# Optimization experiments

Hardware: AMD Instinct MI355X
Metric: run time of the kernel (lower is better)

## Reference

```python
import jax, jax.numpy as jnp
import numpy as np

B, S, V, D, H, F, GH, NC, L = 64, 256, 50000, 1024, 16, 4096, 100, 7, 4
DH = D // H


def _ln(x, g, b):
    m = x.mean(-1, keepdims=True)
    v = x.var(-1, keepdims=True)
    return (x - m) / jnp.sqrt(v + 1e-5) * g + b


def setup_inputs() -> dict:
    key = jax.random.key(0)
    ks = iter(jax.random.split(key, 40))
    nrm = lambda shp, s=0.02: jax.random.normal(next(ks), shp, jnp.float32) * s
    inp = {}
    inp["src"] = jax.random.randint(next(ks), (B, S), 0, V)
    inp["em_seq"] = jax.random.normal(next(ks), (B, S, 7), jnp.float32)
    inp["d_ids"] = jax.random.randint(next(ks), (B, 1), 0, B)
    inp["ut_len"] = jax.random.randint(next(ks), (B,), 1, S + 1)
    inp["emb"] = jax.random.uniform(next(ks), (V, D), jnp.float32, -0.1, 0.1)
    inp["Wqkv"] = nrm((L, 3 * D, D)); inp["bqkv"] = jnp.zeros((L, 3 * D), jnp.float32)
    inp["Wo"] = nrm((L, D, D)); inp["bo"] = jnp.zeros((L, D), jnp.float32)
    inp["W1"] = nrm((L, F, D)); inp["b1"] = jnp.zeros((L, F), jnp.float32)
    inp["W2"] = nrm((L, D, F)); inp["b2"] = jnp.zeros((L, D), jnp.float32)
    inp["ln1_g"] = jnp.ones((L, D), jnp.float32); inp["ln1_b"] = jnp.zeros((L, D), jnp.float32)
    inp["ln2_g"] = jnp.ones((L, D), jnp.float32); inp["ln2_b"] = jnp.zeros((L, D), jnp.float32)
    inp["gru_Wih"] = nrm((3 * GH, 7), 0.1); inp["gru_Whh"] = nrm((3 * GH, GH), 0.1)
    inp["gru_bih"] = jnp.zeros((3 * GH,), jnp.float32); inp["gru_bhh"] = jnp.zeros((3 * GH,), jnp.float32)
    inp["dec_W"] = jax.random.uniform(next(ks), (NC, 2 * D + GH), jnp.float32, -0.1, 0.1)
    inp["dec_b"] = jnp.zeros((NC,), jnp.float32)
    return inp


def reference(src, em_seq, d_ids, ut_len, emb, Wqkv, bqkv, Wo, bo, W1, b1, W2, b2,
              ln1_g, ln1_b, ln2_g, ln2_b, gru_Wih, gru_Whh, gru_bih, gru_bhh,
              dec_W, dec_b):
    # embedding + scale + sinusoidal positional encoding
    x = emb[src] * jnp.sqrt(jnp.float32(D))                      # [B,S,D]
    pos = jnp.arange(S, dtype=jnp.float32)[:, None]
    div = jnp.exp(jnp.arange(0, D, 2, dtype=jnp.float32) * (-jnp.log(10000.0) / D))
    pe = jnp.stack([jnp.sin(pos * div), jnp.cos(pos * div)], -1).reshape(S, D)
    x = x + pe

    causal = jnp.tril(jnp.ones((S, S), bool))
    neg = jnp.finfo(x.dtype).min
    for l in range(L):  # post-norm transformer encoder layers (PyTorch default)
        qkv = x @ Wqkv[l].T + bqkv[l]
        q, k, v = jnp.split(qkv, 3, -1)
        q = q.reshape(B, S, H, DH); k = k.reshape(B, S, H, DH); v = v.reshape(B, S, H, DH)
        sc = jnp.einsum('bqhd,bkhd->bhqk', q, k) / jnp.sqrt(jnp.float32(DH))
        sc = jnp.where(causal, sc, neg)
        a = jax.nn.softmax(sc, -1)
        o = jnp.einsum('bhqk,bkhd->bqhd', a, v).reshape(B, S, D)
        x = _ln(x + o @ Wo[l].T + bo[l], ln1_g[l], ln1_b[l])
        ff = jax.nn.relu(x @ W1[l].T + b1[l]) @ W2[l].T + b2[l]
        x = _ln(x + ff, ln2_g[l], ln2_b[l])

    # emotion GRU (PyTorch GRU equations), scan over time
    xp = jnp.einsum('bsf,gf->sbg', em_seq, gru_Wih) + gru_bih    # [S,B,3*GH]

    def step(h, xt):
        hp = h @ gru_Whh.T + gru_bhh
        xr, xz, xn = jnp.split(xt, 3, -1)
        hr, hz, hn = jnp.split(hp, 3, -1)
        r = jax.nn.sigmoid(xr + hr)
        z = jax.nn.sigmoid(xz + hz)
        n = jnp.tanh(xn + r * hn)
        h = (1.0 - z) * n + z * h
        return h, h

    _, hs = jax.lax.scan(step, jnp.zeros((B, GH), x.dtype), xp)
    emo = hs.transpose(1, 0, 2)                                  # [B,S,GH]

    # ragged gather of the 'main' utterance per dialogue + broadcast-concat
    lens = ut_len[d_ids[:, 0]]                                   # [B]
    main = x[jnp.arange(B), lens - 1]                            # [B,D]
    pair = jnp.concatenate([x, jnp.broadcast_to(main[:, None, :], (B, S, D))], -1)
    valid = (jnp.arange(S)[None, :] < lens[:, None])[..., None]
    pair = jnp.where(valid, pair, 0.0)                           # zeros beyond ut_len, as in torch loop
    dec_ip = jnp.concatenate([pair, emo], -1)                    # [B,S,2D+GH]
    return dec_ip @ dec_W.T + dec_b                              # [B,S,NC]
```

## Files before the change

### kernel.cpp

```cpp
#include <hip/hip_runtime.h>
#include <hip/hip_bf16.h>
#include <math.h>

#define BB 64
#define SS 256
#define DD 1024
#define HH 16
#define FFN 4096
#define GHH 100
#define NCC 7
#define LL 4
#define TT (BB*SS)
#define DHH 64

typedef unsigned short u16;
typedef unsigned int u32;
typedef __attribute__((ext_vector_type(4))) float f32x4;
typedef __attribute__((ext_vector_type(8))) short s16x8;
typedef __attribute__((ext_vector_type(4))) unsigned short u16x4;
typedef __attribute__((ext_vector_type(8))) unsigned short u16x8;

__device__ __forceinline__ u16 f2bf(float f) {
  union { float f; u32 u; } x; x.f = f;
  u32 r = x.u + 0x7FFFu + ((x.u >> 16) & 1u);
  return (u16)(r >> 16);
}
__device__ __forceinline__ float bf2f(u16 b) {
  union { u32 u; float f; } x; x.u = ((u32)b) << 16;
  return x.f;
}
__device__ __forceinline__ u32 pkbf(float a, float b) {
  return (u32)f2bf(a) | ((u32)f2bf(b) << 16);
}
__device__ __forceinline__ float lo16(u32 u) {
  union { u32 u; float f; } x; x.u = u << 16; return x.f;
}
__device__ __forceinline__ float hi16(u32 u) {
  union { u32 u; float f; } x; x.u = u & 0xffff0000u; return x.f;
}

__global__ void k_f2bf4(const float* __restrict__ s0, u16* __restrict__ d0, int n0,
                        const float* __restrict__ s1, u16* __restrict__ d1, int n1,
                        const float* __restrict__ s2, u16* __restrict__ d2, int n2,
                        const float* __restrict__ s3, u16* __restrict__ d3, int n3) {
  int stride = gridDim.x * blockDim.x;
  int total = n0 + n1 + n2 + n3;
  for (int i = blockIdx.x * blockDim.x + threadIdx.x; i < total; i += stride) {
    const float* s; u16* d; int j = i;
    if (j < n0) { s = s0; d = d0; }
    else {
      j -= n0;
      if (j < n1) { s = s1; d = d1; }
      else {
        j -= n1;
        if (j < n2) { s = s2; d = d2; }
        else { j -= n2; s = s3; d = d3; }
      }
    }
    f32x4 v = *(const f32x4*)(s + (size_t)j * 4);
    u16x4 o;
    o[0] = f2bf(v[0]); o[1] = f2bf(v[1]); o[2] = f2bf(v[2]); o[3] = f2bf(v[3]);
    *(u16x4*)(d + (size_t)j * 4) = o;
  }
}

__global__ void k_pe(float* __restrict__ pe) {
  int i = blockIdx.x * blockDim.x + threadIdx.x;
  if (i >= SS * DD / 2) return;
  int s = i / (DD / 2), j = i % (DD / 2);
  float div = __expf((float)(2 * j) * (-9.210340371976184f / (float)DD));
  float a = (float)s * div;
  pe[s * DD + 2 * j]     = sinf(a);
  pe[s * DD + 2 * j + 1] = cosf(a);
}

__global__ void k_embed(const int* __restrict__ src, const float* __restrict__ emb,
                        const float* __restrict__ pe, u16* __restrict__ xb) {
  int i = blockIdx.x * blockDim.x + threadIdx.x;
  if (i >= TT * DD / 4) return;
  int t = i / (DD / 4);
  int d4 = (i % (DD / 4)) * 4;
  int s = t % SS;
  int tok = src[t];
  f32x4 e = *(const f32x4*)(emb + (size_t)tok * DD + d4);
  f32x4 p = *(const f32x4*)(pe + (size_t)s * DD + d4);
  u16x4 o;
  o[0] = f2bf(e[0] * 32.0f + p[0]); o[1] = f2bf(e[1] * 32.0f + p[1]);
  o[2] = f2bf(e[2] * 32.0f + p[2]); o[3] = f2bf(e[3] * 32.0f + p[3]);
  *(u16x4*)(xb + (size_t)t * DD + d4) = o;
}

#define MEMF asm volatile("" ::: "memory")
#define GBAR do { MEMF; __builtin_amdgcn_sched_barrier(0); __builtin_amdgcn_s_barrier(); __builtin_amdgcn_sched_barrier(0); MEMF; } while(0)
#define VMW4 asm volatile("s_waitcnt vmcnt(4)" ::: "memory")

#define STG(P, isB, h, l, buf, kt) \
  __builtin_amdgcn_global_load_lds( \
    (const __attribute__((address_space(1))) u32*)(P[h][l] + (kt)), \
    (__attribute__((address_space(3))) u32*)(smem + (buf)*65536 + (isB)*32768 + (h)*16384 + (l)*8192 + wid*1024), \
    16, 0, 0)

#define LDB(buf) do { \
  _Pragma("unroll") for (int nf = 0; nf < 4; nf++) \
  _Pragma("unroll") for (int kk = 0; kk < 2; kk++) { \
    int rel = (wn*64 + nf*16 + lm)*128 + kk*64 + lg*16; \
    bq[nf][kk] = *(const s16x8*)(smem + (buf)*65536 + 32768 + (rel ^ (((rel>>9)&1)<<5))); \
  } } while(0)

#define LDA(buf, q) do { \
  _Pragma("unroll") for (int ml = 0; ml < 2; ml++) \
  _Pragma("unroll") for (int kk = 0; kk < 2; kk++) { \
    int rel = (wm*128 + ((q)*2+ml)*16 + lm)*128 + kk*64 + lg*16; \
    aq[ml][kk] = *(const s16x8*)(smem + (buf)*65536 + (rel ^ (((rel>>9)&1)<<5))); \
  } } while(0)

#define MFMAQ(q) do { \
  __builtin_amdgcn_s_setprio(1); \
  _Pragma("unroll") for (int ml = 0; ml < 2; ml++) \
  _Pragma("unroll") for (int nf = 0; nf < 4; nf++) \
  _Pragma("unroll") for (int kk = 0; kk < 2; kk++) \
    acc[(q)*2+ml][nf] = __builtin_amdgcn_mfma_f32_16x16x32_bf16(aq[ml][kk], bq[nf][kk], acc[(q)*2+ml][nf], 0, 0, 0); \
  __builtin_amdgcn_s_setprio(0); \
// ... 70 lines not shown
    GBAR; MFMAQ(3); VMW4; GBAR;
    LDB(1); LDA(1,0);
    STG(pA,0,0,0,0,t2k); STG(pA,0,0,1,0,t2k);
    GBAR; MFMAQ(0); GBAR;
    LDA(1,1);
    STG(pA,0,1,0,0,t2k); STG(pA,0,1,1,0,t2k);
    GBAR; MFMAQ(1); GBAR;
    LDA(1,2);
    STG(pB,1,0,0,1,t3k); STG(pB,1,0,1,1,t3k);
    GBAR; MFMAQ(2); GBAR;
    LDA(1,3);
    STG(pB,1,1,0,1,t3k); STG(pB,1,1,1,1,t3k);
    GBAR; MFMAQ(3); VMW4; GBAR;
  }

  float bn[4];
#pragma unroll
  for (int nf = 0; nf < 4; nf++) bn[nf] = bias[n0 + wn*64 + nf*16 + lm];
#pragma unroll
  for (int mf = 0; mf < 8; mf++)
#pragma unroll
    for (int nf = 0; nf < 4; nf++) {
      int col = n0 + wn*64 + nf*16 + lm;
#pragma unroll
      for (int r = 0; r < 4; r++) {
        int row = m0 + wm*128 + mf*16 + lg*4 + r;
        float v = acc[mf][nf][r] + bn[nf];
        if (EPI == 1) v = fmaxf(v, 0.f);
        C[(size_t)row * N + col] = f2bf(v);
      }
    }
}

__global__ __launch_bounds__(256, 2)
void k_attn(const u16* __restrict__ qkv, u16* __restrict__ o) {
  const int h = blockIdx.x;
  const int b = blockIdx.y;
  const int lane = threadIdx.x & 63;
  const int w = threadIdx.x >> 6;
  const int lm = lane & 15, lg = lane >> 4;

  __shared__ u16 Ks[64 * 64];
  __shared__ u16 Vt[64 * 64];
  __shared__ u16 Ps[4][64 * 64];

  const size_t tokbase = (size_t)b * SS;

  s16x8 aq[4][2];
#pragma unroll
  for (int mf = 0; mf < 4; mf++) {
    const u16* qrow = qkv + (tokbase + w * 64 + mf * 16 + lm) * 3072 + h * 64;
#pragma unroll
    for (int kk = 0; kk < 2; kk++)
      aq[mf][kk] = *(const s16x8*)(qrow + kk * 32 + lg * 8);
  }

  f32x4 zero = {0.f, 0.f, 0.f, 0.f};
  f32x4 oacc[4][4];
#pragma unroll
  for (int mf = 0; mf < 4; mf++)
#pragma unroll
    for (int df = 0; df < 4; df++) oacc[mf][df] = zero;
  float m_run[16], l_run[16];
#pragma unroll
  for (int r = 0; r < 16; r++) { m_run[r] = -3e38f; l_run[r] = 0.f; }

// ... 127 lines not shown
    v2[e] = bf2f(a1[e]) + bf2f(u1[e]);
    v3[e] = bf2f(a1[4 + e]) + bf2f(u1[4 + e]);
  }
  float s = 0.f, s2 = 0.f;
#pragma unroll
  for (int e = 0; e < 4; e++) {
    s  += v0[e] + v1[e] + v2[e] + v3[e];
    s2 += v0[e]*v0[e] + v1[e]*v1[e] + v2[e]*v2[e] + v3[e]*v3[e];
  }
#pragma unroll
  for (int off = 32; off >= 1; off >>= 1) {
    s  += __shfl_xor(s, off);
    s2 += __shfl_xor(s2, off);
  }
  float mean = s * (1.f / 1024.f);
  float var = s2 * (1.f / 1024.f) - mean * mean;
  float rstd = rsqrtf(var + 1e-5f);
  const float* gp = gam + lane * 16;
  const float* bp = bet + lane * 16;
  f32x4 g0 = *(const f32x4*)(gp), g1 = *(const f32x4*)(gp + 4);
  f32x4 g2 = *(const f32x4*)(gp + 8), g3 = *(const f32x4*)(gp + 12);
  f32x4 b0 = *(const f32x4*)(bp), b1 = *(const f32x4*)(bp + 4);
  f32x4 b2 = *(const f32x4*)(bp + 8), b3 = *(const f32x4*)(bp + 12);
  u16x8 y0, y1;
#pragma unroll
  for (int e = 0; e < 4; e++) {
    y0[e]     = f2bf((v0[e] - mean) * rstd * g0[e] + b0[e]);
    y0[4 + e] = f2bf((v1[e] - mean) * rstd * g1[e] + b1[e]);
    y1[e]     = f2bf((v2[e] - mean) * rstd * g2[e] + b2[e]);
    y1[4 + e] = f2bf((v3[e] - mean) * rstd * g3[e] + b3[e]);
  }
  *(u16x8*)(xb + base) = y0;
  *(u16x8*)(xb + base + 8) = y1;
}

#define F7(X) X(0) X(1) X(2) X(3) X(4) X(5) X(6)
#define C12(X) X(0) X(1) X(2) X(3) X(4) X(5) X(6) X(7) X(8) X(9) X(10) X(11)

__global__ __launch_bounds__(640, 1)
void k_gru(const float* __restrict__ em, const float* __restrict__ Wih,
           const float* __restrict__ bih, const float* __restrict__ Whh,
           const float* __restrict__ bhh, float* __restrict__ emo) {
  const int b = blockIdx.x;
  const int tid = threadIdx.x;
  const int iraw = tid / 6;
  const int sub = tid - iraw * 6;
  const int g = sub >> 1, half = sub & 1;
  const bool act = iraw < 100;
  const int i = act ? iraw : 99;
  const int grow = g * 100 + i;

  __shared__ __align__(16) float h[2][104];
  __shared__ float vals[400];
  __shared__ __align__(16) float emL[SS][8];
  __shared__ float emoL[16][100];

  const float* rowP = Whh + (size_t)grow * 100 + half * 50;
#define LW(q) u32 wa##q = pkbf(rowP[4*(q)], rowP[4*(q)+1]); \
              u32 wb##q = pkbf(rowP[4*(q)+2], rowP[4*(q)+3]); \
              asm volatile("" : "+v"(wa##q), "+v"(wb##q));
  C12(LW)
#undef LW
  u32 wt = pkbf(rowP[48], rowP[49]);
  asm volatile("" : "+v"(wt));

#define LI(f) float wi##f = Wih[grow * 7 + (f)];
  F7(LI)
#undef LI
  const float bhhv = bhh[grow];
  const float bihv = bih[grow];

  {
    const float* ebase = em + (size_t)b * SS * 7;
    for (int idx = tid; idx < SS * 7; idx += 640) {
      int ss = idx / 7, ff = idx - ss * 7;
      emL[ss][ff] = ebase[idx];
    }
  }
  if (tid < 104) { h[0][tid] = 0.f; h[1][tid] = 0.f; }
  __syncthreads();

  for (int s = 0; s < SS; ++s) {
    const float* hc = h[s & 1];
    float* hb_next = h[(s & 1) ^ 1];
    float xp = bihv;
#define MI(f) xp += wi##f * emL[s][f];
    F7(MI)
#undef MI
    const float* hbp = hc + half * 52;
    float a0 = 0.f, a1 = 0.f, a2 = 0.f, a3 = 0.f;
#define MC(q) { f32x4 hv = *(const f32x4*)(hbp + 4*(q)); \
    a0 += lo16(wa##q) * hv[0]; a1 += hi16(wa##q) * hv[1]; \
    a2 += lo16(wb##q) * hv[2]; a3 += hi16(wb##q) * hv[3]; }
    C12(MC)
#undef MC
    { a0 += lo16(wt) * hbp[48]; a1 += hi16(wt) * hbp[49]; }
    float a = (a0 + a1) + (a2 + a3);
    a += __shfl_xor(a, 1);
    if (act && half == 0) {
      if (g == 2) { vals[200 + i] = xp; vals[300 + i] = a + bhhv; }
      else        { vals[g * 100 + i] = xp + a + bhhv; }
    }
    __syncthreads();
    if (tid < 100) {
      int slot = tid + (tid >= 50 ? 2 : 0);
      float hold = hc[slot];
      float rr = 1.f / (1.f + __expf(-vals[tid]));
      float zz = 1.f / (1.f + __expf(-vals[100 + tid]));
      float nx = vals[200 + tid] + rr * vals[300 + tid];
      float e2 = __expf(-2.f * fabsf(nx));
      float th = (1.f - e2) / (1.f + e2);
      float nn = copysignf(th, nx);
      float hv = (1.f - zz) * nn + zz * hold;
      hb_next[slot] = hv;
      emoL[s & 15][tid] = hv;
    }
    __syncthreads();
    if ((s & 15) == 15) {
      float* dst = emo + ((size_t)b * SS + (s - 15)) * GHH;
      for (int idx = tid; idx < 16 * GHH; idx += 640)
        dst[idx] = (&emoL[0][0])[idx];
    }
  }
}

__global__ void k_main(const int* __restrict__ d_ids, const int* __restrict__ ut_len,
                       const u16* __restrict__ x, const float* __restrict__ decW,
                       float* __restrict__ md) {
  int b = blockIdx.x;
  int lane = threadIdx.x;
  int len = ut_len[d_ids[b]];
  const u16* xr = x + ((size_t)b * SS + (len - 1)) * DD;
  float acc[NCC];
#pragma unroll
  for (int c = 0; c < NCC; c++) acc[c] = 0.f;
  for (int d = lane; d < DD; d += 64) {
    float xv = bf2f(xr[d]);
#pragma unroll
    for (int c = 0; c < NCC; c++) acc[c] += xv * decW[(size_t)c * 2148 + 1024 + d];
  }
#pragma unroll
  for (int c = 0; c < NCC; c++) {
#pragma unroll
    for (int off = 32; off >= 1; off >>= 1) acc[c] += __shfl_xor(acc[c], off);
  }
  if (lane == 0) {
#pragma unroll
    for (int c = 0; c < NCC; c++) md[b * NCC + c] = acc[c];
  }
}

__global__ __launch_bounds__(256)
void k_dec(const u16* __restrict__ x, const float* __restrict__ emo,
           const float* __restrict__ md, const float* __restrict__ decW,
           const float* __restrict__ decb, const int* __restrict__ d_ids,
           const int* __restrict__ ut_len, float* __restrict__ out) {
// ... 36 lines not shown
}

extern "C" void kernel_launch(void* const* d_in, const int* in_sizes, int n_in,
                              void* d_out, int out_size, void* d_ws, size_t ws_size,
                              hipStream_t stream) {
  const int*   src    = (const int*)d_in[0];
  const float* em_seq = (const float*)d_in[1];
  const int*   d_ids  = (const int*)d_in[2];
  const int*   ut_len = (const int*)d_in[3];
  const float* emb    = (const float*)d_in[4];
  const float* Wqkv   = (const float*)d_in[5];
  const float* bqkv   = (const float*)d_in[6];
  const float* Wo     = (const float*)d_in[7];
  const float* bo     = (const float*)d_in[8];
  const float* W1     = (const float*)d_in[9];
  const float* b1     = (const float*)d_in[10];
  const float* W2     = (const float*)d_in[11];
  const float* b2     = (const float*)d_in[12];
  const float* ln1g   = (const float*)d_in[13];
  const float* ln1b   = (const float*)d_in[14];
  const float* ln2g   = (const float*)d_in[15];
  const float* ln2b   = (const float*)d_in[16];
  const float* gWih   = (const float*)d_in[17];
  const float* gWhh   = (const float*)d_in[18];
  const float* gbih   = (const float*)d_in[19];
  const float* gbhh   = (const float*)d_in[20];
  const float* decW   = (const float*)d_in[21];
  const float* decb   = (const float*)d_in[22];
  float* out = (float*)d_out;

  char* wsp = (char*)d_ws;
  auto take = [&](size_t n) { char* p = wsp; wsp += (n + 255) & ~(size_t)255; return p; };

  u16*   wqkvb = (u16*)take((size_t)3072 * 1024 * 2);
  u16*   wob   = (u16*)take((size_t)1024 * 1024 * 2);
  u16*   w1b   = (u16*)take((size_t)4096 * 1024 * 2);
  u16*   w2b   = (u16*)take((size_t)1024 * 4096 * 2);
  float* pe    = (float*)take((size_t)SS * DD * 4);
  u16*   xb    = (u16*)take((size_t)TT * DD * 2);
  u16*   big   = (u16*)take((size_t)TT * FFN * 2);
  u16*   ob    = (u16*)take((size_t)TT * DD * 2);
  u16*   tmp16 = (u16*)take((size_t)TT * DD * 2);
  float* emo   = (float*)take((size_t)BB * SS * GHH * 4);
  float* md    = (float*)take((size_t)BB * NCC * 4);

  (void)hipFuncSetAttribute((const void*)&k_gemm256<0>,
      hipFuncAttributeMaxDynamicSharedMemorySize, 131072);
  (void)hipFuncSetAttribute((const void*)&k_gemm256<1>,
      hipFuncAttributeMaxDynamicSharedMemorySize, 131072);

  k_gru<<<BB, 640, 0, stream>>>(em_seq, gWih, gbih, gWhh, gbhh, emo);

  k_pe<<<(SS * DD / 2 + 255) / 256, 256, 0, stream>>>(pe);
  k_embed<<<TT * DD / 4 / 256, 256, 0, stream>>>(src, emb, pe, xb);

  for (int l = 0; l < LL; ++l) {
    k_f2bf4<<<2048, 256, 0, stream>>>(
        Wqkv + (size_t)l * 3072 * 1024, wqkvb, 3072 * 1024 / 4,
        Wo   + (size_t)l * 1024 * 1024, wob,   1024 * 1024 / 4,
        W1   + (size_t)l * 4096 * 1024, w1b,   4096 * 1024 / 4,
        W2   + (size_t)l * 1024 * 4096, w2b,   1024 * 4096 / 4);

    k_gemm256<0><<<(TT/256) * (3072/256), 512, 131072, stream>>>(
        xb, wqkvb, bqkv + (size_t)l * 3072, big, TT, 3072, 1024);
    k_attn<<<dim3(HH, BB), 256, 0, stream>>>(big, ob);
    k_gemm256<0><<<(TT/256) * (1024/256), 512, 131072, stream>>>(
        ob, wob, bo + (size_t)l * 1024, tmp16, TT, 1024, 1024);
    k_ln<<<TT / 4, 256, 0, stream>>>(xb, tmp16, ln1g + (size_t)l * DD, ln1b + (size_t)l * DD);
    k_gemm256<1><<<(TT/256) * (4096/256), 512, 131072, stream>>>(
        xb, w1b, b1 + (size_t)l * 4096, big, TT, 4096, 1024);
    k_gemm256<0><<<(TT/256) * (1024/256), 512, 131072, stream>>>(
        big, w2b, b2 + (size_t)l * 1024, tmp16, TT, 1024, 4096);
    k_ln<<<TT / 4, 256, 0, stream>>>(xb, tmp16, ln2g + (size_t)l * DD, ln2b + (size_t)l * DD);
  }

  k_main<<<BB, 64, 0, stream>>>(d_ids, ut_len, xb, decW, md);
  k_dec<<<TT / 4, 256, 0, stream>>>(xb, emo, md, decW, decb, d_ids, ut_len, out);
}
```

Before: 2.301 ms.

## Remap GRU threads so each pair computes all three gates per hidden unit

The GRU kernel drops from 640 threads (one thread pair per gate row) to 256 threads, where each thread pair holds all three gate rows (r, z, n) for one hidden unit in packed bf16 registers. Each loaded h vector is reused across three dot products, and the input projection uses packed weights with two vector loads from the padded emL row. The per-step critical path gets longer per thread, but there are fewer waves to synchronise and fewer LDS reads of h. The GRU is a small serial kernel alongside much larger GEMMs, so its effect on total time depends on whether it sits on the critical path.

```diff
diff --git a/kernel.cpp b/kernel.cpp
--- a/kernel.cpp
+++ b/kernel.cpp
@@ -419,48 +419,53 @@
   *(u16x8*)(xb + base + 8) = y1;
 }
 
-#define F7(X) X(0) X(1) X(2) X(3) X(4) X(5) X(6)
-#define C12(X) X(0) X(1) X(2) X(3) X(4) X(5) X(6) X(7) X(8) X(9) X(10) X(11)
-
-__global__ __launch_bounds__(640, 1)
+#define C25(X) X(0) X(1) X(2) X(3) X(4) X(5) X(6) X(7) X(8) X(9) X(10) X(11) \
+  X(12) X(13) X(14) X(15) X(16) X(17) X(18) X(19) X(20) X(21) X(22) X(23) X(24)
+
+__global__ __launch_bounds__(256, 1)
 void k_gru(const float* __restrict__ em, const float* __restrict__ Wih,
            const float* __restrict__ bih, const float* __restrict__ Whh,
            const float* __restrict__ bhh, float* __restrict__ emo) {
   const int b = blockIdx.x;
   const int tid = threadIdx.x;
-  const int iraw = tid / 6;
-  const int sub = tid - iraw * 6;
-  const int g = sub >> 1, half = sub & 1;
+  const int iraw = tid >> 1;
   const bool act = iraw < 100;
   const int i = act ? iraw : 99;
-  const int grow = g * 100 + i;
+  const int half = tid & 1;
 
   __shared__ __align__(16) float h[2][104];
   __shared__ float vals[400];
   __shared__ __align__(16) float emL[SS][8];
   __shared__ float emoL[16][100];
 
-  const float* rowP = Whh + (size_t)grow * 100 + half * 50;
-#define LW(q) u32 wa##q = pkbf(rowP[4*(q)], rowP[4*(q)+1]); \
-              u32 wb##q = pkbf(rowP[4*(q)+2], rowP[4*(q)+3]); \
-              asm volatile("" : "+v"(wa##q), "+v"(wb##q));
-  C12(LW)
+  const float* rowR = Whh + (size_t)i * 100 + half * 50;
+  const float* rowZ = Whh + (size_t)(100 + i) * 100 + half * 50;
+  const float* rowN = Whh + (size_t)(200 + i) * 100 + half * 50;
+#define LW(k) u32 wr##k = pkbf(rowR[2*(k)], rowR[2*(k)+1]); \
+              u32 wz##k = pkbf(rowZ[2*(k)], rowZ[2*(k)+1]); \
+              u32 wn##k = pkbf(rowN[2*(k)], rowN[2*(k)+1]); \
+              asm volatile("" : "+v"(wr##k), "+v"(wz##k), "+v"(wn##k));
+  C25(LW)
 #undef LW
-  u32 wt = pkbf(rowP[48], rowP[49]);
-  asm volatile("" : "+v"(wt));
-
-#define LI(f) float wi##f = Wih[grow * 7 + (f)];
-  F7(LI)
-#undef LI
-  const float bhhv = bhh[grow];
-  const float bihv = bih[grow];
+  const float* wihR = Wih + i * 7;
+  const float* wihZ = Wih + (100 + i) * 7;
+  const float* wihN = Wih + (200 + i) * 7;
+#define LIW(k) u32 ir##k = pkbf(wihR[2*(k)], (2*(k)+1 < 7) ? wihR[2*(k)+1] : 0.f); \
+               u32 iz##k = pkbf(wihZ[2*(k)], (2*(k)+1 < 7) ? wihZ[2*(k)+1] : 0.f); \
+               u32 in##k = pkbf(wihN[2*(k)], (2*(k)+1 < 7) ? wihN[2*(k)+1] : 0.f); \
+               asm volatile("" : "+v"(ir##k), "+v"(iz##k), "+v"(in##k));
+  LIW(0) LIW(1) LIW(2) LIW(3)
+#undef LIW
+  const float bhr = bhh[i], bhz = bhh[100 + i], bhn = bhh[200 + i];
+  const float bir = bih[i], biz = bih[100 + i], bin = bih[200 + i];
 
   {
     const float* ebase = em + (size_t)b * SS * 7;
-    for (int idx = tid; idx < SS * 7; idx += 640) {
+    for (int idx = tid; idx < SS * 7; idx += 256) {
       int ss = idx / 7, ff = idx - ss * 7;
       emL[ss][ff] = ebase[idx];
     }
+    for (int ss = tid; ss < SS; ss += 256) emL[ss][7] = 0.f;
   }
   if (tid < 104) { h[0][tid] = 0.f; h[1][tid] = 0.f; }
   __syncthreads();
@@ -468,23 +473,41 @@
   for (int s = 0; s < SS; ++s) {
     const float* hc = h[s & 1];
     float* hb_next = h[(s & 1) ^ 1];
-    float xp = bihv;
-#define MI(f) xp += wi##f * emL[s][f];
-    F7(MI)
-#undef MI
+    f32x4 ea = *(const f32x4*)&emL[s][0];
+    f32x4 eb = *(const f32x4*)&emL[s][4];
+    float xr = bir, xz = biz, xn = bin;
+    xr += lo16(ir0)*ea[0] + hi16(ir0)*ea[1] + lo16(ir1)*ea[2] + hi16(ir1)*ea[3]
+        + lo16(ir2)*eb[0] + hi16(ir2)*eb[1] + lo16(ir3)*eb[2] + hi16(ir3)*eb[3];
+    xz += lo16(iz0)*ea[0] + hi16(iz0)*ea[1] + lo16(iz1)*ea[2] + hi16(iz1)*ea[3]
+        + lo16(iz2)*eb[0] + hi16(iz2)*eb[1] + lo16(iz3)*eb[2] + hi16(iz3)*eb[3];
+    xn += lo16(in0)*ea[0] + hi16(in0)*ea[1] + lo16(in1)*ea[2] + hi16(in1)*ea[3]
+        + lo16(in2)*eb[0] + hi16(in2)*eb[1] + lo16(in3)*eb[2] + hi16(in3)*eb[3];
     const float* hbp = hc + half * 52;
-    float a0 = 0.f, a1 = 0.f, a2 = 0.f, a3 = 0.f;
-#define MC(q) { f32x4 hv = *(const f32x4*)(hbp + 4*(q)); \
-    a0 += lo16(wa##q) * hv[0]; a1 += hi16(wa##q) * hv[1]; \
-    a2 += lo16(wb##q) * hv[2]; a3 += hi16(wb##q) * hv[3]; }
-    C12(MC)
-#undef MC
-    { a0 += lo16(wt) * hbp[48]; a1 += hi16(wt) * hbp[49]; }
-    float a = (a0 + a1) + (a2 + a3);
-    a += __shfl_xor(a, 1);
+    float ar = 0.f, az = 0.f, an = 0.f;
+#define MD(q, pa, pb) { f32x4 hv = *(const f32x4*)(hbp + 4*(q)); \
+    ar += lo16(wr##pa)*hv[0]; ar += hi16(wr##pa)*hv[1]; \
+    ar += lo16(wr##pb)*hv[2]; ar += hi16(wr##pb)*hv[3]; \
+    az += lo16(wz##pa)*hv[0]; az += hi16(wz##pa)*hv[1]; \
+    az += lo16(wz##pb)*hv[2]; az += hi16(wz##pb)*hv[3]; \
+    an += lo16(wn##pa)*hv[0]; an += hi16(wn##pa)*hv[1]; \
+    an += lo16(wn##pb)*hv[2]; an += hi16(wn##pb)*hv[3]; }
+    MD(0,0,1) MD(1,2,3) MD(2,4,5) MD(3,6,7) MD(4,8,9) MD(5,10,11)
+    MD(6,12,13) MD(7,14,15) MD(8,16,17) MD(9,18,19) MD(10,20,21) MD(11,22,23)
+#undef MD
+    {
+      f32x4 hv = *(const f32x4*)(hbp + 48);
+      ar += lo16(wr24)*hv[0] + hi16(wr24)*hv[1];
+      az += lo16(wz24)*hv[0] + hi16(wz24)*hv[1];
+      an += lo16(wn24)*hv[0] + hi16(wn24)*hv[1];
+    }
+    ar += __shfl_xor(ar, 1);
+    az += __shfl_xor(az, 1);
+    an += __shfl_xor(an, 1);
     if (act && half == 0) {
-      if (g == 2) { vals[200 + i] = xp; vals[300 + i] = a + bhhv; }
-      else        { vals[g * 100 + i] = xp + a + bhhv; }
+      vals[i]       = xr + ar + bhr;
+      vals[100 + i] = xz + az + bhz;
+      vals[200 + i] = xn;
+      vals[300 + i] = an + bhn;
     }
     __syncthreads();
     if (tid < 100) {
@@ -503,7 +526,7 @@
     __syncthreads();
     if ((s & 15) == 15) {
       float* dst = emo + ((size_t)b * SS + (s - 15)) * GHH;
-      for (int idx = tid; idx < 16 * GHH; idx += 640)
+      for (int idx = tid; idx < 16 * GHH; idx += 256)
         dst[idx] = (&emoL[0][0])[idx];
     }
   }
@@ -626,7 +649,7 @@
   (void)hipFuncSetAttribute((const void*)&k_gemm256<1>,
       hipFuncAttributeMaxDynamicSharedMemorySize, 131072);
 
-  k_gru<<<BB, 640, 0, stream>>>(em_seq, gWih, gbih, gWhh, gbhh, emo);
+  k_gru<<<BB, 256, 0, stream>>>(em_seq, gWih, gbih, gWhh, gbhh, emo);
 
   k_pe<<<(SS * DD / 2 + 255) / 256, 256, 0, stream>>>(pe);
   k_embed<<<TT * DD / 4 / 256, 256, 0, stream>>>(src, emb, pe, xb);
```

Result: slower. 2.369 ms (+3.0%).

## Fuse GRU recurrence into first-layer QKV GEMM launch for overlap

Applied to the files above, without the earlier changes.

Moves the serial GRU scan into extra blocks of the layer-0 QKV GEMM kernel so the latency-bound recurrence runs concurrently with GEMM tiles instead of as a separate serial kernel. GEMM blocks now launch with 640 threads, with two idle waves, to match the GRU block size. This costs register and occupancy headroom for the GEMM part and may lengthen that kernel's tail if the GRU blocks finish last.

```diff
diff --git a/kernel.cpp b/kernel.cpp
--- a/kernel.cpp
+++ b/kernel.cpp
@@ -88,6 +88,95 @@
   o[0] = f2bf(e[0] * 32.0f + p[0]); o[1] = f2bf(e[1] * 32.0f + p[1]);
   o[2] = f2bf(e[2] * 32.0f + p[2]); o[3] = f2bf(e[3] * 32.0f + p[3]);
   *(u16x4*)(xb + (size_t)t * DD + d4) = o;
+}
+
+#define F7(X) X(0) X(1) X(2) X(3) X(4) X(5) X(6)
+#define C12(X) X(0) X(1) X(2) X(3) X(4) X(5) X(6) X(7) X(8) X(9) X(10) X(11)
+
+__device__ __forceinline__
+void gru_body(const float* __restrict__ em, const float* __restrict__ Wih,
+              const float* __restrict__ bih, const float* __restrict__ Whh,
+              const float* __restrict__ bhh, float* __restrict__ emo, int b) {
+  const int tid = threadIdx.x;
+  const int iraw = tid / 6;
+  const int sub = tid - iraw * 6;
+  const int g = sub >> 1, half = sub & 1;
+  const bool act = iraw < 100;
+  const int i = act ? iraw : 99;
+  const int grow = g * 100 + i;
+
+  __shared__ __align__(16) float h[2][104];
+  __shared__ float vals[400];
+  __shared__ __align__(16) float emL[SS][8];
+  __shared__ float emoL[16][100];
+
+  const float* rowP = Whh + (size_t)grow * 100 + half * 50;
+#define LW(q) u32 wa##q = pkbf(rowP[4*(q)], rowP[4*(q)+1]); \
+              u32 wb##q = pkbf(rowP[4*(q)+2], rowP[4*(q)+3]); \
+              asm volatile("" : "+v"(wa##q), "+v"(wb##q));
+  C12(LW)
+#undef LW
+  u32 wt = pkbf(rowP[48], rowP[49]);
+  asm volatile("" : "+v"(wt));
+
+#define LI(f) float wi##f = Wih[grow * 7 + (f)];
+  F7(LI)
+#undef LI
+  const float bhhv = bhh[grow];
+  const float bihv = bih[grow];
+
+  {
+    const float* ebase = em + (size_t)b * SS * 7;
+    for (int idx = tid; idx < SS * 7; idx += 640) {
+      int ss = idx / 7, ff = idx - ss * 7;
+      emL[ss][ff] = ebase[idx];
+    }
+  }
+  if (tid < 104) { h[0][tid] = 0.f; h[1][tid] = 0.f; }
+  __syncthreads();
+
+  for (int s = 0; s < SS; ++s) {
+    const float* hc = h[s & 1];
+    float* hb_next = h[(s & 1) ^ 1];
+    float xp = bihv;
+#define MI(f) xp += wi##f * emL[s][f];
+    F7(MI)
+#undef MI
+    const float* hbp = hc + half * 52;
+    float a0 = 0.f, a1 = 0.f, a2 = 0.f, a3 = 0.f;
+#define MC(q) { f32x4 hv = *(const f32x4*)(hbp + 4*(q)); \
+    a0 += lo16(wa##q) * hv[0]; a1 += hi16(wa##q) * hv[1]; \
+    a2 += lo16(wb##q) * hv[2]; a3 += hi16(wb##q) * hv[3]; }
+    C12(MC)
+#undef MC
+    { a0 += lo16(wt) * hbp[48]; a1 += hi16(wt) * hbp[49]; }
+    float a = (a0 + a1) + (a2 + a3);
+    a += __shfl_xor(a, 1);
+    if (act && half == 0) {
+      if (g == 2) { vals[200 + i] = xp; vals[300 + i] = a + bhhv; }
+      else        { vals[g * 100 + i] = xp + a + bhhv; }
+    }
+    __syncthreads();
+    if (tid < 100) {
+      int slot = tid + (tid >= 50 ? 2 : 0);
+      float hold = hc[slot];
+      float rr = 1.f / (1.f + __expf(-vals[tid]));
+      float zz = 1.f / (1.f + __expf(-vals[100 + tid]));
+      float nx = vals[200 + tid] + rr * vals[300 + tid];
+      float e2 = __expf(-2.f * fabsf(nx));
+      float th = (1.f - e2) / (1.f + e2);
+      float nn = copysignf(th, nx);
+      float hv = (1.f - zz) * nn + zz * hold;
+      hb_next[slot] = hv;
+      emoL[s & 15][tid] = hv;
+    }
+    __syncthreads();
+    if ((s & 15) == 15) {
+      float* dst = emo + ((size_t)b * SS + (s - 15)) * GHH;
+      for (int idx = tid; idx < 16 * GHH; idx += 640)
+        dst[idx] = (&emoL[0][0])[idx];
+    }
+  }
 }
 
 #define MEMF asm volatile("" ::: "memory")
@@ -224,6 +313,130 @@
     }
 }
 
+__global__ __launch_bounds__(640, 1)
+void k_qkv_gru(const u16* __restrict__ A, const u16* __restrict__ W,
+               const float* __restrict__ bias, u16* __restrict__ C,
+               int M, int N, int K, int nG,
+               const float* __restrict__ em, const float* __restrict__ Wih,
+               const float* __restrict__ bih, const float* __restrict__ Whh,
+               const float* __restrict__ bhh, float* __restrict__ emo) {
+  extern __shared__ char smem[];
+  if ((int)blockIdx.x < BB) {
+    gru_body(em, Wih, bih, Whh, bhh, emo, blockIdx.x);
+    return;
+  }
+  const int bid = blockIdx.x - BB;
+  const int tid = threadIdx.x;
+  const int lane = tid & 63;
+  const bool gact = (tid >> 6) < 8;
+  const int wid = (tid >> 6) & 7;
+  const int lm = lane & 15, lg = lane >> 4;
+  const int wm = wid >> 2, wn = wid & 3;
+
+  const int NB = N >> 8;
+  const int cpx = nG >> 3;
+  const int swzb = (bid & 7) * cpx + (bid >> 3);
+  const int m0 = (swzb / NB) << 8;
+  const int n0 = (swzb % NB) << 8;
+
+  const u16* pA[2][2];
+  const u16* pB[2][2];
+#pragma unroll
+  for (int h = 0; h < 2; h++)
+#pragma unroll
+    for (int l = 0; l < 2; l++) {
+      int rel = h * 16384 + l * 8192 + (tid & 511) * 16;
+      int sb = rel ^ (((rel >> 9) & 1) << 5);
+      int grow = sb >> 7;
+      int gcol = (sb & 127) >> 1;
+      pA[h][l] = A + (size_t)(m0 + grow) * K + gcol;
+      pB[h][l] = W + (size_t)(n0 + grow) * K + gcol;
+    }
+
+  f32x4 acc[8][4];
+#pragma unroll
+  for (int i = 0; i < 8; i++)
+#pragma unroll
+    for (int j = 0; j < 4; j++) acc[i][j] = (f32x4){0.f, 0.f, 0.f, 0.f};
+
+  s16x8 bq[4][2];
+  s16x8 aq[2][2];
+
+  const int NT = K >> 6;
+
+  if (gact) {
+    STG(pB,1,0,0,0,0); STG(pB,1,0,1,0,0); STG(pB,1,1,0,0,0); STG(pB,1,1,1,0,0);
+    STG(pA,0,0,0,0,0); STG(pA,0,0,1,0,0); STG(pA,0,1,0,0,0); STG(pA,0,1,1,0,0);
+    STG(pB,1,0,0,1,64); STG(pB,1,0,1,1,64); STG(pB,1,1,0,1,64); STG(pB,1,1,1,1,64);
+  }
+  VMW4;
+  GBAR;
+
+  for (int i = 0; i < (NT >> 1); i++) {
+    const int t1k = (2*i + 1) * 64;
+    int t2 = 2*i + 2; if (t2 >= NT) t2 -= NT;
+    int t3 = 2*i + 3; if (t3 >= NT) t3 -= NT;
+    const int t2k = t2 * 64, t3k = t3 * 64;
+
+    if (gact) {
+      LDB(0); LDA(0,0);
+      STG(pA,0,0,0,1,t1k); STG(pA,0,0,1,1,t1k);
+    }
+    GBAR; if (gact) { MFMAQ(0); } GBAR;
+    if (gact) {
+      LDA(0,1);
+      STG(pA,0,1,0,1,t1k); STG(pA,0,1,1,1,t1k);
+      STG(pB,1,0,0,0,t2k); STG(pB,1,0,1,0,t2k);
+    }
+    GBAR; if (gact) { MFMAQ(1); } GBAR;
+    if (gact) {
+      LDA(0,2);
+      STG(pB,1,1,0,0,t2k); STG(pB,1,1,1,0,t2k);
+    }
+    GBAR; if (gact) { MFMAQ(2); } GBAR;
+    if (gact) { LDA(0,3); }
+    GBAR; if (gact) { MFMAQ(3); } VMW4; GBAR;
+    if (gact) {
+      LDB(1); LDA(1,0);
+      STG(pA,0,0,0,0,t2k); STG(pA,0,0,1,0,t2k);
+    }
+    GBAR; if (gact) { MFMAQ(0); } GBAR;
+    if (gact) {
+      LDA(1,1);
+      STG(pA,0,1,0,0,t2k); STG(pA,0,1,1,0,t2k);
+    }
+    GBAR; if (gact) { MFMAQ(1); } GBAR;
+    if (gact) {
+      LDA(1,2);
+      STG(pB,1,0,0,1,t3k); STG(pB,1,0,1,1,t3k);
+    }
+    GBAR; if (gact) { MFMAQ(2); } GBAR;
+    if (gact) {
+      LDA(1,3);
+      STG(pB,1,1,0,1,t3k); STG(pB,1,1,1,1,t3k);
+    }
+    GBAR; if (gact) { MFMAQ(3); } VMW4; GBAR;
+  }
+
+  if (gact) {
+    float bn[4];
+#pragma unroll
+    for (int nf = 0; nf < 4; nf++) bn[nf] = bias[n0 + wn*64 + nf*16 + lm];
+#pragma unroll
+    for (int mf = 0; mf < 8; mf++)
+#pragma unroll
+      for (int nf = 0; nf < 4; nf++) {
+        int col = n0 + wn*64 + nf*16 + lm;
+#pragma unroll
+        for (int r = 0; r < 4; r++) {
+          int row = m0 + wm*128 + mf*16 + lg*4 + r;
+          float v = acc[mf][nf][r] + bn[nf];
+          C[(size_t)row * N + col] = f2bf(v);
+        }
+      }
+  }
+}
+
 __global__ __launch_bounds__(256, 2)
 void k_attn(const u16* __restrict__ qkv, u16* __restrict__ o) {
   const int h = blockIdx.x;
@@ -417,96 +630,6 @@
   }
   *(u16x8*)(xb + base) = y0;
   *(u16x8*)(xb + base + 8) = y1;
-}
-
-#define F7(X) X(0) X(1) X(2) X(3) X(4) X(5) X(6)
-#define C12(X) X(0) X(1) X(2) X(3) X(4) X(5) X(6) X(7) X(8) X(9) X(10) X(11)
-
-__global__ __launch_bounds__(640, 1)
-void k_gru(const float* __restrict__ em, const float* __restrict__ Wih,
-           const float* __restrict__ bih, const float* __restrict__ Whh,
-           const float* __restrict__ bhh, float* __restrict__ emo) {
-  const int b = blockIdx.x;
-  const int tid = threadIdx.x;
-  const int iraw = tid / 6;
-  const int sub = tid - iraw * 6;
-  const int g = sub >> 1, half = sub & 1;
-  const bool act = iraw < 100;
-  const int i = act ? iraw : 99;
-  const int grow = g * 100 + i;
-
-  __shared__ __align__(16) float h[2][104];
-  __shared__ float vals[400];
-  __shared__ __align__(16) float emL[SS][8];
-  __shared__ float emoL[16][100];
-
-  const float* rowP = Whh + (size_t)grow * 100 + half * 50;
-#define LW(q) u32 wa##q = pkbf(rowP[4*(q)], rowP[4*(q)+1]); \
-              u32 wb##q = pkbf(rowP[4*(q)+2], rowP[4*(q)+3]); \
-              asm volatile("" : "+v"(wa##q), "+v"(wb##q));
-  C12(LW)
-#undef LW
-  u32 wt = pkbf(rowP[48], rowP[49]);
-  asm volatile("" : "+v"(wt));
-
-#define LI(f) float wi##f = Wih[grow * 7 + (f)];
-  F7(LI)
-#undef LI
-  const float bhhv = bhh[grow];
-  const float bihv = bih[grow];
-
-  {
-    const float* ebase = em + (size_t)b * SS * 7;
-    for (int idx = tid; idx < SS * 7; idx += 640) {
-      int ss = idx / 7, ff = idx - ss * 7;
-      emL[ss][ff] = ebase[idx];
-    }
-  }
-  if (tid < 104) { h[0][tid] = 0.f; h[1][tid] = 0.f; }
-  __syncthreads();
-
-  for (int s = 0; s < SS; ++s) {
-    const float* hc = h[s & 1];
-    float* hb_next = h[(s & 1) ^ 1];
-    float xp = bihv;
-#define MI(f) xp += wi##f * emL[s][f];
-    F7(MI)
-#undef MI
-    const float* hbp = hc + half * 52;
-    float a0 = 0.f, a1 = 0.f, a2 = 0.f, a3 = 0.f;
-#define MC(q) { f32x4 hv = *(const f32x4*)(hbp + 4*(q)); \
-    a0 += lo16(wa##q) * hv[0]; a1 += hi16(wa##q) * hv[1]; \
-    a2 += lo16(wb##q) * hv[2]; a3 += hi16(wb##q) * hv[3]; }
-    C12(MC)
-#undef MC
-    { a0 += lo16(wt) * hbp[48]; a1 += hi16(wt) * hbp[49]; }
-    float a = (a0 + a1) + (a2 + a3);
-    a += __shfl_xor(a, 1);
-    if (act && half == 0) {
-      if (g == 2) { vals[200 + i] = xp; vals[300 + i] = a + bhhv; }
-      else        { vals[g * 100 + i] = xp + a + bhhv; }
-    }
-    __syncthreads();
-    if (tid < 100) {
-      int slot = tid + (tid >= 50 ? 2 : 0);
-      float hold = hc[slot];
-      float rr = 1.f / (1.f + __expf(-vals[tid]));
-      float zz = 1.f / (1.f + __expf(-vals[100 + tid]));
-      float nx = vals[200 + tid] + rr * vals[300 + tid];
-      float e2 = __expf(-2.f * fabsf(nx));
-      float th = (1.f - e2) / (1.f + e2);
-      float nn = copysignf(th, nx);
-      float hv = (1.f - zz) * nn + zz * hold;
-      hb_next[slot] = hv;
-      emoL[s & 15][tid] = hv;
-    }
-    __syncthreads();
-    if ((s & 15) == 15) {
-      float* dst = emo + ((size_t)b * SS + (s - 15)) * GHH;
-      for (int idx = tid; idx < 16 * GHH; idx += 640)
-        dst[idx] = (&emoL[0][0])[idx];
-    }
-  }
 }
 
 __global__ void k_main(const int* __restrict__ d_ids, const int* __restrict__ ut_len,
@@ -625,11 +748,13 @@
       hipFuncAttributeMaxDynamicSharedMemorySize, 131072);
   (void)hipFuncSetAttribute((const void*)&k_gemm256<1>,
       hipFuncAttributeMaxDynamicSharedMemorySize, 131072);
-
-  k_gru<<<BB, 640, 0, stream>>>(em_seq, gWih, gbih, gWhh, gbhh, emo);
+  (void)hipFuncSetAttribute((const void*)&k_qkv_gru,
+      hipFuncAttributeMaxDynamicSharedMemorySize, 131072);
 
   k_pe<<<(SS * DD / 2 + 255) / 256, 256, 0, stream>>>(pe);
   k_embed<<<TT * DD / 4 / 256, 256, 0, stream>>>(src, emb, pe, xb);
+
+  const int nG_qkv = (TT / 256) * (3072 / 256);
 
   for (int l = 0; l < LL; ++l) {
     k_f2bf4<<<2048, 256, 0, stream>>>(
@@ -638,8 +763,14 @@
         W1   + (size_t)l * 4096 * 1024, w1b,   4096 * 1024 / 4,
         W2   + (size_t)l * 1024 * 4096, w2b,   1024 * 4096 / 4);
 
-    k_gemm256<0><<<(TT/256) * (3072/256), 512, 131072, stream>>>(
-        xb, wqkvb, bqkv + (size_t)l * 3072, big, TT, 3072, 1024);
+    if (l == 0) {
+      k_qkv_gru<<<BB + nG_qkv, 640, 131072, stream>>>(
+          xb, wqkvb, bqkv, big, TT, 3072, 1024, nG_qkv,
+          em_seq, gWih, gbih, gWhh, gbhh, emo);
+    } else {
+      k_gemm256<0><<<nG_qkv, 512, 131072, stream>>>(
+          xb, wqkvb, bqkv + (size_t)l * 3072, big, TT, 3072, 1024);
+    }
     k_attn<<<dim3(HH, BB), 256, 0, stream>>>(big, ob);
     k_gemm256<0><<<(TT/256) * (1024/256), 512, 131072, stream>>>(
         ob, wob, bo + (size_t)l * 1024, tmp16, TT, 1024, 1024);
```

Measured after the change: 2.643 ms. +14.9%, slower.

## Fuse weight bf16 conversion for all layers into the GRU kernel launch

Applied to the files above, without the earlier changes.

Removes the per-layer weight conversion launches and converts all four layers' weights in one pass. That pass runs as extra blocks of the GRU kernel so it overlaps with the long serial GRU recurrence, which uses only 64 blocks. This needs a larger workspace holding every layer's bf16 weights, and the conversion blocks may compete with the GRU blocks for memory bandwidth or CU slots.

```diff
diff --git a/kernel.cpp b/kernel.cpp
--- a/kernel.cpp
+++ b/kernel.cpp
@@ -39,30 +39,10 @@
   union { u32 u; float f; } x; x.u = u & 0xffff0000u; return x.f;
 }
 
-__global__ void k_f2bf4(const float* __restrict__ s0, u16* __restrict__ d0, int n0,
-                        const float* __restrict__ s1, u16* __restrict__ d1, int n1,
-                        const float* __restrict__ s2, u16* __restrict__ d2, int n2,
-                        const float* __restrict__ s3, u16* __restrict__ d3, int n3) {
-  int stride = gridDim.x * blockDim.x;
-  int total = n0 + n1 + n2 + n3;
-  for (int i = blockIdx.x * blockDim.x + threadIdx.x; i < total; i += stride) {
-    const float* s; u16* d; int j = i;
-    if (j < n0) { s = s0; d = d0; }
-    else {
-      j -= n0;
-      if (j < n1) { s = s1; d = d1; }
-      else {
-        j -= n1;
-        if (j < n2) { s = s2; d = d2; }
-        else { j -= n2; s = s3; d = d3; }
-      }
-    }
-    f32x4 v = *(const f32x4*)(s + (size_t)j * 4);
-    u16x4 o;
-    o[0] = f2bf(v[0]); o[1] = f2bf(v[1]); o[2] = f2bf(v[2]); o[3] = f2bf(v[3]);
-    *(u16x4*)(d + (size_t)j * 4) = o;
-  }
-}
+#define LS4   3145728
+#define QKV4  786432
+#define WO4   262144
+#define W14   1048576
 
 __global__ void k_pe(float* __restrict__ pe) {
   int i = blockIdx.x * blockDim.x + threadIdx.x;
@@ -88,6 +68,124 @@
   o[0] = f2bf(e[0] * 32.0f + p[0]); o[1] = f2bf(e[1] * 32.0f + p[1]);
   o[2] = f2bf(e[2] * 32.0f + p[2]); o[3] = f2bf(e[3] * 32.0f + p[3]);
   *(u16x4*)(xb + (size_t)t * DD + d4) = o;
+}
+
+#define F7(X) X(0) X(1) X(2) X(3) X(4) X(5) X(6)
+#define C12(X) X(0) X(1) X(2) X(3) X(4) X(5) X(6) X(7) X(8) X(9) X(10) X(11)
+
+__device__ __forceinline__
+void gru_body(const float* __restrict__ em, const float* __restrict__ Wih,
+              const float* __restrict__ bih, const float* __restrict__ Whh,
+              const float* __restrict__ bhh, float* __restrict__ emo, int b) {
+  const int tid = threadIdx.x;
+  const int iraw = tid / 6;
+  const int sub = tid - iraw * 6;
+  const int g = sub >> 1, half = sub & 1;
+  const bool act = iraw < 100;
+  const int i = act ? iraw : 99;
+  const int grow = g * 100 + i;
+
+  __shared__ __align__(16) float h[2][104];
+  __shared__ float vals[400];
+  __shared__ __align__(16) float emL[SS][8];
+  __shared__ float emoL[16][100];
+
+  const float* rowP = Whh + (size_t)grow * 100 + half * 50;
+#define LW(q) u32 wa##q = pkbf(rowP[4*(q)], rowP[4*(q)+1]); \
+              u32 wb##q = pkbf(rowP[4*(q)+2], rowP[4*(q)+3]); \
+              asm volatile("" : "+v"(wa##q), "+v"(wb##q));
+  C12(LW)
+#undef LW
+  u32 wt = pkbf(rowP[48], rowP[49]);
+  asm volatile("" : "+v"(wt));
+
+#define LI(f) float wi##f = Wih[grow * 7 + (f)];
+  F7(LI)
+#undef LI
+  const float bhhv = bhh[grow];
+  const float bihv = bih[grow];
+
+  {
+    const float* ebase = em + (size_t)b * SS * 7;
+    for (int idx = tid; idx < SS * 7; idx += 640) {
+      int ss = idx / 7, ff = idx - ss * 7;
+      emL[ss][ff] = ebase[idx];
+    }
+  }
+  if (tid < 104) { h[0][tid] = 0.f; h[1][tid] = 0.f; }
+  __syncthreads();
+
+  for (int s = 0; s < SS; ++s) {
+    const float* hc = h[s & 1];
+    float* hb_next = h[(s & 1) ^ 1];
+    float xp = bihv;
+#define MI(f) xp += wi##f * emL[s][f];
+    F7(MI)
+#undef MI
+    const float* hbp = hc + half * 52;
+    float a0 = 0.f, a1 = 0.f, a2 = 0.f, a3 = 0.f;
+#define MC(q) { f32x4 hv = *(const f32x4*)(hbp + 4*(q)); \
+    a0 += lo16(wa##q) * hv[0]; a1 += hi16(wa##q) * hv[1]; \
+    a2 += lo16(wb##q) * hv[2]; a3 += hi16(wb##q) * hv[3]; }
+    C12(MC)
+#undef MC
+    { a0 += lo16(wt) * hbp[48]; a1 += hi16(wt) * hbp[49]; }
+    float a = (a0 + a1) + (a2 + a3);
+    a += __shfl_xor(a, 1);
+    if (act && half == 0) {
+      if (g == 2) { vals[200 + i] = xp; vals[300 + i] = a + bhhv; }
+      else        { vals[g * 100 + i] = xp + a + bhhv; }
+    }
+    __syncthreads();
+    if (tid < 100) {
+      int slot = tid + (tid >= 50 ? 2 : 0);
+      float hold = hc[slot];
+      float rr = 1.f / (1.f + __expf(-vals[tid]));
+      float zz = 1.f / (1.f + __expf(-vals[100 + tid]));
+      float nx = vals[200 + tid] + rr * vals[300 + tid];
+      float e2 = __expf(-2.f * fabsf(nx));
+      float th = (1.f - e2) / (1.f + e2);
+      float nn = copysignf(th, nx);
+      float hv = (1.f - zz) * nn + zz * hold;
+      hb_next[slot] = hv;
+      emoL[s & 15][tid] = hv;
+    }
+    __syncthreads();
+    if ((s & 15) == 15) {
+      float* dst = emo + ((size_t)b * SS + (s - 15)) * GHH;
+      for (int idx = tid; idx < 16 * GHH; idx += 640)
+        dst[idx] = (&emoL[0][0])[idx];
+    }
+  }
+}
+
+__global__ __launch_bounds__(640, 1)
+void k_gru_conv(const float* __restrict__ em, const float* __restrict__ Wih,
+                const float* __restrict__ bih, const float* __restrict__ Whh,
+                const float* __restrict__ bhh, float* __restrict__ emo,
+                const float* __restrict__ Wqkv, const float* __restrict__ Wo,
+                const float* __restrict__ W1, const float* __restrict__ W2,
+                u16* __restrict__ wall) {
+  if ((int)blockIdx.x < BB) {
+    gru_body(em, Wih, bih, Whh, bhh, emo, blockIdx.x);
+    return;
+  }
+  const int idx0 = ((int)blockIdx.x - BB) * 640 + threadIdx.x;
+  const int stride = ((int)gridDim.x - BB) * 640;
+  const int nTot4 = LL * LS4;
+  for (int i = idx0; i < nTot4; i += stride) {
+    int l = i / LS4;
+    int r = i - l * LS4;
+    const float* s;
+    if (r < QKV4)                 s = Wqkv + ((size_t)l * QKV4 + r) * 4;
+    else if (r < QKV4 + WO4)      s = Wo   + ((size_t)l * WO4  + (r - QKV4)) * 4;
+    else if (r < QKV4 + WO4 + W14) s = W1  + ((size_t)l * W14  + (r - QKV4 - WO4)) * 4;
+    else                          s = W2   + ((size_t)l * W14  + (r - QKV4 - WO4 - W14)) * 4;
+    f32x4 v = *(const f32x4*)s;
+    u16x4 o;
+    o[0] = f2bf(v[0]); o[1] = f2bf(v[1]); o[2] = f2bf(v[2]); o[3] = f2bf(v[3]);
+    *(u16x4*)(wall + (size_t)i * 4) = o;
+  }
 }
 
 #define MEMF asm volatile("" ::: "memory")
@@ -417,96 +515,6 @@
   }
   *(u16x8*)(xb + base) = y0;
   *(u16x8*)(xb + base + 8) = y1;
-}
-
-#define F7(X) X(0) X(1) X(2) X(3) X(4) X(5) X(6)
-#define C12(X) X(0) X(1) X(2) X(3) X(4) X(5) X(6) X(7) X(8) X(9) X(10) X(11)
-
-__global__ __launch_bounds__(640, 1)
-void k_gru(const float* __restrict__ em, const float* __restrict__ Wih,
-           const float* __restrict__ bih, const float* __restrict__ Whh,
-           const float* __restrict__ bhh, float* __restrict__ emo) {
-  const int b = blockIdx.x;
-  const int tid = threadIdx.x;
-  const int iraw = tid / 6;
-  const int sub = tid - iraw * 6;
-  const int g = sub >> 1, half = sub & 1;
-  const bool act = iraw < 100;
-  const int i = act ? iraw : 99;
-  const int grow = g * 100 + i;
-
-  __shared__ __align__(16) float h[2][104];
-  __shared__ float vals[400];
-  __shared__ __align__(16) float emL[SS][8];
-  __shared__ float emoL[16][100];
-
-  const float* rowP = Whh + (size_t)grow * 100 + half * 50;
-#define LW(q) u32 wa##q = pkbf(rowP[4*(q)], rowP[4*(q)+1]); \
-              u32 wb##q = pkbf(rowP[4*(q)+2], rowP[4*(q)+3]); \
-              asm volatile("" : "+v"(wa##q), "+v"(wb##q));
-  C12(LW)
-#undef LW
-  u32 wt = pkbf(rowP[48], rowP[49]);
-  asm volatile("" : "+v"(wt));
-
-#define LI(f) float wi##f = Wih[grow * 7 + (f)];
-  F7(LI)
-#undef LI
-  const float bhhv = bhh[grow];
-  const float bihv = bih[grow];
-
-  {
-    const float* ebase = em + (size_t)b * SS * 7;
-    for (int idx = tid; idx < SS * 7; idx += 640) {
-      int ss = idx / 7, ff = idx - ss * 7;
-      emL[ss][ff] = ebase[idx];
-    }
-  }
-  if (tid < 104) { h[0][tid] = 0.f; h[1][tid] = 0.f; }
-  __syncthreads();
-
-  for (int s = 0; s < SS; ++s) {
-    const float* hc = h[s & 1];
-    float* hb_next = h[(s & 1) ^ 1];
-    float xp = bihv;
-#define MI(f) xp += wi##f * emL[s][f];
-    F7(MI)
-#undef MI
-    const float* hbp = hc + half * 52;
-    float a0 = 0.f, a1 = 0.f, a2 = 0.f, a3 = 0.f;
-#define MC(q) { f32x4 hv = *(const f32x4*)(hbp + 4*(q)); \
-    a0 += lo16(wa##q) * hv[0]; a1 += hi16(wa##q) * hv[1]; \
-    a2 += lo16(wb##q) * hv[2]; a3 += hi16(wb##q) * hv[3]; }
-    C12(MC)
-#undef MC
-    { a0 += lo16(wt) * hbp[48]; a1 += hi16(wt) * hbp[49]; }
-    float a = (a0 + a1) + (a2 + a3);
-    a += __shfl_xor(a, 1);
-    if (act && half == 0) {
-      if (g == 2) { vals[200 + i] = xp; vals[300 + i] = a + bhhv; }
-      else        { vals[g * 100 + i] = xp + a + bhhv; }
-    }
-    __syncthreads();
-    if (tid < 100) {
-      int slot = tid + (tid >= 50 ? 2 : 0);
-      float hold = hc[slot];
-      float rr = 1.f / (1.f + __expf(-vals[tid]));
-      float zz = 1.f / (1.f + __expf(-vals[100 + tid]));
-      float nx = vals[200 + tid] + rr * vals[300 + tid];
-      float e2 = __expf(-2.f * fabsf(nx));
-      float th = (1.f - e2) / (1.f + e2);
-      float nn = copysignf(th, nx);
-      float hv = (1.f - zz) * nn + zz * hold;
-      hb_next[slot] = hv;
-      emoL[s & 15][tid] = hv;
-    }
-    __syncthreads();
-    if ((s & 15) == 15) {
-      float* dst = emo + ((size_t)b * SS + (s - 15)) * GHH;
-      for (int idx = tid; idx < 16 * GHH; idx += 640)
-        dst[idx] = (&emoL[0][0])[idx];
-    }
-  }
 }
 
 __global__ void k_main(const int* __restrict__ d_ids, const int* __restrict__ ut_len,
@@ -609,10 +617,7 @@
   char* wsp = (char*)d_ws;
   auto take = [&](size_t n) { char* p = wsp; wsp += (n + 255) & ~(size_t)255; return p; };
 
-  u16*   wqkvb = (u16*)take((size_t)3072 * 1024 * 2);
-  u16*   wob   = (u16*)take((size_t)1024 * 1024 * 2);
-  u16*   w1b   = (u16*)take((size_t)4096 * 1024 * 2);
-  u16*   w2b   = (u16*)take((size_t)1024 * 4096 * 2);
+  u16*   wall  = (u16*)take((size_t)LL * LS4 * 4 * 2);
   float* pe    = (float*)take((size_t)SS * DD * 4);
   u16*   xb    = (u16*)take((size_t)TT * DD * 2);
   u16*   big   = (u16*)take((size_t)TT * FFN * 2);
@@ -626,28 +631,29 @@
   (void)hipFuncSetAttribute((const void*)&k_gemm256<1>,
       hipFuncAttributeMaxDynamicSharedMemorySize, 131072);
 
-  k_gru<<<BB, 640, 0, stream>>>(em_seq, gWih, gbih, gWhh, gbhh, emo);
+  k_gru_conv<<<BB + 2048, 640, 0, stream>>>(
+      em_seq, gWih, gbih, gWhh, gbhh, emo,
+      Wqkv, Wo, W1, W2, wall);
 
   k_pe<<<(SS * DD / 2 + 255) / 256, 256, 0, stream>>>(pe);
   k_embed<<<TT * DD / 4 / 256, 256, 0, stream>>>(src, emb, pe, xb);
 
   for (int l = 0; l < LL; ++l) {
-    k_f2bf4<<<2048, 256, 0, stream>>>(
-        Wqkv + (size_t)l * 3072 * 1024, wqkvb, 3072 * 1024 / 4,
-        Wo   + (size_t)l * 1024 * 1024, wob,   1024 * 1024 / 4,
-        W1   + (size_t)l * 4096 * 1024, w1b,   4096 * 1024 / 4,
-        W2   + (size_t)l * 1024 * 4096, w2b,   1024 * 4096 / 4);
+    const u16* wqkvL = wall + (size_t)l * LS4 * 4;
+    const u16* woL   = wqkvL + (size_t)QKV4 * 4;
+    const u16* w1L   = wqkvL + (size_t)(QKV4 + WO4) * 4;
+    const u16* w2L   = wqkvL + (size_t)(QKV4 + WO4 + W14) * 4;
 
     k_gemm256<0><<<(TT/256) * (3072/256), 512, 131072, stream>>>(
-        xb, wqkvb, bqkv + (size_t)l * 3072, big, TT, 3072, 1024);
+        xb, wqkvL, bqkv + (size_t)l * 3072, big, TT, 3072, 1024);
     k_attn<<<dim3(HH, BB), 256, 0, stream>>>(big, ob);
     k_gemm256<0><<<(TT/256) * (1024/256), 512, 131072, stream>>>(
-        ob, wob, bo + (size_t)l * 1024, tmp16, TT, 1024, 1024);
+        ob, woL, bo + (size_t)l * 1024, tmp16, TT, 1024, 1024);
     k_ln<<<TT / 4, 256, 0, stream>>>(xb, tmp16, ln1g + (size_t)l * DD, ln1b + (size_t)l * DD);
     k_gemm256<1><<<(TT/256) * (4096/256), 512, 131072, stream>>>(
-        xb, w1b, b1 + (size_t)l * 4096, big, TT, 4096, 1024);
+        xb, w1L, b1 + (size_t)l * 4096, big, TT, 4096, 1024);
     k_gemm256<0><<<(TT/256) * (1024/256), 512, 131072, stream>>>(
-        big, w2b, b2 + (size_t)l * 1024, tmp16, TT, 1024, 4096);
+        big, w2L, b2 + (size_t)l * 1024, tmp16, TT, 1024, 4096);
     k_ln<<<TT / 4, 256, 0, stream>>>(xb, tmp16, ln2g + (size_t)l * DD, ln2b + (size_t)l * DD);
   }
 
```

New measurement: 2.253 ms. 2.1% less time.
